# Performance work log

Measured on AMD Instinct MI355X. Metric: run time of the kernel, lower is better.

Reference implementation:

```python
import jax, jax.numpy as jnp
import numpy as np

D = 512        # input_dim
T = 64         # n_trees
DEPTH = 3
NI = 2 ** DEPTH - 1   # 7 internal nodes
NL = 2 ** DEPTH       # 8 leaves
PPT = NI * D + NI + NL * 2   # params per tree
TOT = PPT * T + T            # + tree_weights
HID = 64


def setup_inputs() -> dict:
    key = jax.random.key(0)
    ks = jax.random.split(key, 10)
    w = lambda k, s: jax.random.normal(k, s, jnp.float32) * 0.05  # xavier-ish small gain
    return {
        "X_train": jax.random.normal(ks[0], (8192, D), jnp.float32),
        "X_test": jax.random.normal(ks[1], (32768, D), jnp.float32),
        "y_train": jax.random.randint(ks[2], (8192,), 0, 2, jnp.int64),
        "W1": w(ks[3], (HID, D)), "b1": jnp.zeros(HID), "g1": jnp.ones(HID), "be1": jnp.zeros(HID),
        "W2": w(ks[4], (HID, HID)), "b2": jnp.zeros(HID),
        "H1": w(ks[5], (2 * HID, HID)), "hb1": jnp.zeros(2 * HID),
        "g2": jnp.ones(2 * HID), "be2": jnp.zeros(2 * HID),
        "H2": w(ks[6], (2 * HID, 2 * HID)), "hb2": jnp.zeros(2 * HID),
        "H3": w(ks[7], (TOT, 2 * HID)), "hb3": jnp.zeros(TOT),
    }


def _ln(x, g, b, eps=1e-5):
    m = x.mean(-1, keepdims=True)
    v = ((x - m) ** 2).mean(-1, keepdims=True)
    return (x - m) / jnp.sqrt(v + eps) * g + b


def reference(X_train, X_test, y_train, W1, b1, g1, be1, W2, b2,
              H1, hb1, g2, be2, H2, hb2, H3, hb3):
    # --- hypernet: data encoder + param generator (Dropout is eval=identity) ---
    h = jax.nn.relu(_ln(X_train @ W1.T + b1, g1, be1))
    h = jax.nn.relu(h @ W2.T + b2)
    c = h.mean(axis=0)                              # [HID] context
    u = jax.nn.relu(_ln(c @ H1.T + hb1, g2, be2))
    u = jax.nn.relu(u @ H2.T + hb2)
    params = u @ H3.T + hb3                         # [TOT]

    # --- parse per-tree params (sequential layout) ---
    rows = params[: T * PPT].reshape(T, PPT)
    sw = rows[:, : NI * D].reshape(T, NI, D)        # split weights
    sb = rows[:, NI * D: NI * D + NI]               # split bias [T, NI]
    ll = rows[:, NI * D + NI:].reshape(T, NL, 2)    # leaf logits
    tw = params[T * PPT:]                           # tree weights [T]

    # --- soft decision trees, all trees/nodes batched ---
    # sigmoid split prob for every (sample, tree, internal node); temperature=1
    p = jax.nn.sigmoid(jnp.einsum('bd,tnd->btn', X_test, sw) + sb[None])  # [B,T,NI]
    B = X_test.shape[0]
    lp = jnp.ones((B, T, 1), X_test.dtype)
    for d in range(DEPTH):                          # unrolled fixed-depth traversal
        s = 2 ** d - 1                              # heap offset of level d
        pd = p[:, :, s: s + 2 ** d]                 # [B,T,2^d]
        lp = jnp.stack([lp * (1 - pd), lp * pd], axis=-1).reshape(B, T, 2 ** (d + 1))
    # original code adds leaf contributions twice (main loop + cleanup loop)
    lp = lp * 2.0                                   # [B,T,NL]

    leaf_dist = jax.nn.softmax(ll, axis=-1)         # [T,NL,2]
    out_t = jnp.einsum('btl,tlc->btc', lp, leaf_dist)
    w = jax.nn.softmax(tw, axis=0)                  # [T]
    return jnp.einsum('btc,t->bc', out_t, w)        # [B,2]
```

## Files before the change

kernel.cpp:

```cpp
#include <hip/hip_runtime.h>
#include <hip/hip_bf16.h>

#define DD 512
#define HIDN 64
#define NTREE 64
#define NIN 7
#define PPTC 3607
#define TOTP 230912
#define SWROWS 448

typedef __attribute__((ext_vector_type(8))) short bf16x8;
typedef __attribute__((ext_vector_type(4))) float f32x4;
typedef __attribute__((ext_vector_type(8))) _Float16 h16x8;

__device__ __forceinline__ unsigned short f2bf(float f) {
  unsigned u = __float_as_uint(f);
  unsigned r = (u + 0x7FFFu + ((u >> 16) & 1u)) >> 16;
  return (unsigned short)r;
}
__device__ __forceinline__ float bf2f(unsigned short h) {
  return __uint_as_float(((unsigned)h) << 16);
}
__device__ __forceinline__ float sigmoidf_(float x) {
  return 1.0f / (1.0f + __expf(-x));
}
__device__ __forceinline__ uint2 pack_bf16x4(float4 v) {
  uint2 pk;
  pk.x = (unsigned)f2bf(v.x) | ((unsigned)f2bf(v.y) << 16);
  pk.y = (unsigned)f2bf(v.z) | ((unsigned)f2bf(v.w) << 16);
  return pk;
}

__global__ __launch_bounds__(256) void k_train(
    const float* __restrict__ Xtr, const float* __restrict__ W1,
    const float* __restrict__ b1, const float* __restrict__ g1,
    const float* __restrict__ be1, const float* __restrict__ W2,
    const float* __restrict__ b2, float* __restrict__ c_accum)
{
  __shared__ __align__(16) char smem[49408];
  char* Xc  = smem;
  char* W1c = smem + 16384;
  char* Hl  = smem + 32768;
  char* W2l = smem + 40960;
  float* cpart = (float*)(smem + 49152);

  const int tid = threadIdx.x;
  const int lane = tid & 63;
  const int wv = tid >> 6;
  const int l15 = lane & 15;
  const int gq = lane >> 4;
  const int rb0 = blockIdx.x * 64;

#pragma unroll
  for (int s = 0; s < 4; ++s) {
    int fidx = tid + s * 256;
    int n = fidx >> 4, kq = fidx & 15;
    float4 v = ((const float4*)W2)[n * 16 + kq];
    uint2 pk = pack_bf16x4(v);
    int off = n * 128 + kq * 8; off ^= (n & 7) << 4;
    *(uint2*)(W2l + off) = pk;
  }
  if (tid < 64) cpart[tid] = 0.0f;

  f32x4 acc1[4];
#pragma unroll
  for (int nt = 0; nt < 4; ++nt) { f32x4 z = {0.f,0.f,0.f,0.f}; acc1[nt] = z; }

  for (int kc = 0; kc < 4; ++kc) {
    __syncthreads();
#pragma unroll
    for (int s = 0; s < 8; ++s) {
      int idx = tid + s * 256;
      int m = idx >> 5, kq = idx & 31;
      float4 v = ((const float4*)Xtr)[(rb0 + m) * 128 + kc * 32 + kq];
      uint2 pk = pack_bf16x4(v);
      int off = m * 256 + kq * 8; off ^= (m & 7) << 4;
      *(uint2*)(Xc + off) = pk;
      float4 w = ((const float4*)W1)[m * 128 + kc * 32 + kq];
      uint2 pw = pack_bf16x4(w);
      *(uint2*)(W1c + off) = pw;
    }
    __syncthreads();
#pragma unroll
    for (int ks = 0; ks < 4; ++ks) {
      int mrow = wv * 16 + l15;
      int aoff = mrow * 256 + ks * 64 + gq * 16; aoff ^= (mrow & 7) << 4;
      bf16x8 afr = *(const bf16x8*)(Xc + aoff);
#pragma unroll
      for (int nt = 0; nt < 4; ++nt) {
        int n = nt * 16 + l15;
        int boff = n * 256 + ks * 64 + gq * 16; boff ^= (n & 7) << 4;
        bf16x8 bfr = *(const bf16x8*)(W1c + boff);
        acc1[nt] = __builtin_amdgcn_mfma_f32_16x16x32_bf16(afr, bfr, acc1[nt], 0, 0, 0);
      }
    }
  }

  float b1v[4], g1v[4], be1v[4], b2v[4];
#pragma unroll
  for (int nt = 0; nt < 4; ++nt) {
    int c = nt * 16 + l15;
    b1v[nt] = b1[c]; g1v[nt] = g1[c]; be1v[nt] = be1[c]; b2v[nt] = b2[c];
  }
  float yv[4][4], s_[4], q_[4];
#pragma unroll
  for (int i = 0; i < 4; ++i) {
    float s = 0.f, q = 0.f;
#pragma unroll
    for (int nt = 0; nt < 4; ++nt) {
      float y = acc1[nt][i] + b1v[nt];
      yv[nt][i] = y; s += y; q += y * y;
    }
    s_[i] = s; q_[i] = q;
  }
#pragma unroll
  for (int off = 1; off < 16; off <<= 1) {
#pragma unroll
    for (int i = 0; i < 4; ++i) {
      s_[i] += __shfl_xor(s_[i], off);
      q_[i] += __shfl_xor(q_[i], off);
    }
  }
  char* Hw = Hl + wv * 2048;
#pragma unroll
  for (int i = 0; i < 4; ++i) {
    float m = s_[i] * (1.0f / 64.0f);
    float var = q_[i] * (1.0f / 64.0f) - m * m;
    float rstd = rsqrtf(var + 1e-5f);
    int mrow = gq * 4 + i;
#pragma unroll
    for (int nt = 0; nt < 4; ++nt) {
      float h = (yv[nt][i] - m) * rstd * g1v[nt] + be1v[nt];
      h = fmaxf(h, 0.0f);
      int col = nt * 16 + l15;
      int off2 = mrow * 128 + col * 2; off2 ^= (mrow & 7) << 4;
      *(unsigned short*)(Hw + off2) = f2bf(h);
    }
  }
  __syncthreads();

  f32x4 acc2[4];
#pragma unroll
  for (int nt = 0; nt < 4; ++nt) { f32x4 z = {0.f,0.f,0.f,0.f}; acc2[nt] = z; }
#pragma unroll
  for (int ks = 0; ks < 2; ++ks) {
    int aoff = l15 * 128 + ks * 64 + gq * 16; aoff ^= (l15 & 7) << 4;
    bf16x8 afr = *(const bf16x8*)(Hw + aoff);
#pragma unroll
    for (int nt = 0; nt < 4; ++nt) {
      int n = nt * 16 + l15;
      int boff = n * 128 + ks * 64 + gq * 16; boff ^= (n & 7) << 4;
      bf16x8 bfr = *(const bf16x8*)(W2l + boff);
      acc2[nt] = __builtin_amdgcn_mfma_f32_16x16x32_bf16(afr, bfr, acc2[nt], 0, 0, 0);
    }
  }
  float cs[4];
#pragma unroll
  for (int nt = 0; nt < 4; ++nt) {
    float s = 0.f;
#pragma unroll
    for (int i = 0; i < 4; ++i) {
      float z = acc2[nt][i] + b2v[nt];
      s += fmaxf(z, 0.0f);
    }
    cs[nt] = s;
  }
#pragma unroll
  for (int nt = 0; nt < 4; ++nt) {
    cs[nt] += __shfl_xor(cs[nt], 16);
    cs[nt] += __shfl_xor(cs[nt], 32);
  }
  if (lane < 16) {
#pragma unroll
    for (int nt = 0; nt < 4; ++nt) atomicAdd(&cpart[nt * 16 + l15], cs[nt]);
  }
  __syncthreads();
  if (tid < 64) atomicAdd(&c_accum[tid], cpart[tid]);
}

__global__ __launch_bounds__(128) void k_head(
    const float* __restrict__ c_accum,
    const float* __restrict__ H1, const float* __restrict__ hb1,
    const float* __restrict__ g2, const float* __restrict__ be2,
    const float* __restrict__ H2, const float* __restrict__ hb2,
    float* __restrict__ u2out)
{
  __shared__ float clds[64];
  __shared__ float u1lds[128];
  __shared__ float red[4];
  int tid = threadIdx.x;
  if (tid < 64) clds[tid] = c_accum[tid] * (1.0f / 8192.0f);
  __syncthreads();
  float acc = hb1[tid];
  for (int k = 0; k < 64; ++k) acc += clds[k] * H1[tid * 64 + k];
  float s = acc, q = acc * acc;
#pragma unroll
  for (int off = 1; off < 64; off <<= 1) { s += __shfl_xor(s, off); q += __shfl_xor(q, off); }
  int wv = tid >> 6;
  if ((tid & 63) == 0) { red[wv * 2] = s; red[wv * 2 + 1] = q; }
  __syncthreads();
  float S = red[0] + red[2], Q = red[1] + red[3];
  float m = S * (1.0f / 128.0f);
  float var = Q * (1.0f / 128.0f) - m * m;
  float rstd = rsqrtf(var + 1e-5f);
  float u1 = fmaxf((acc - m) * rstd * g2[tid] + be2[tid], 0.0f);
  u1lds[tid] = u1;
  __syncthreads();
  float a2 = hb2[tid];
  for (int k = 0; k < 128; ++k) a2 += u1lds[k] * H2[tid * 128 + k];
  u2out[tid] = fmaxf(a2, 0.0f);
}

__global__ __launch_bounds__(256) void k_params(
    const float* __restrict__ H3, const float* __restrict__ hb3,
    const float* __restrict__ u2,
    unsigned short* __restrict__ Bsw, float* __restrict__ sb,
    float* __restrict__ ll, float* __restrict__ tw)
{
  __shared__ float u2l[128];
  int tid = threadIdx.x;
  if (tid < 128) u2l[tid] = u2[tid];
  __syncthreads();
  int row = blockIdx.x * 64 + (tid >> 2);
  int sub = tid & 3;
  float acc = 0.0f;
  const float4* H4 = (const float4*)H3;
#pragma unroll
  for (int j = 0; j < 8; ++j) {
    int f = j * 4 + sub;
    float4 v = H4[row * 32 + f];
    acc += v.x * u2l[f * 4] + v.y * u2l[f * 4 + 1] + v.z * u2l[f * 4 + 2] + v.w * u2l[f * 4 + 3];
  }
  acc += __shfl_xor(acc, 1);
  acc += __shfl_xor(acc, 2);
  if (sub == 0) {
    float val = acc + hb3[row];
    if (row >= 230848) {
      tw[row - 230848] = val;
    } else {
      int t = row / PPTC;
      int r = row - t * PPTC;
      if (r < 3584) {
        int n = r >> 9, d = r & 511;
        Bsw[(t * 7 + n) * 512 + d] = f2bf(val);
      } else if (r < 3591) {
        sb[t * 7 + (r - 3584)] = val;
      } else {
        ll[t * 16 + (r - 3591)] = val;
      }
    }
  }
}

__global__ __launch_bounds__(64) void k_qprep(
    const float* __restrict__ ll, const float* __restrict__ tw,
    float* __restrict__ q)
{
  int t = threadIdx.x;
  float x = tw[t];
  float m = x;
#pragma unroll
  for (int off = 1; off < 64; off <<= 1) m = fmaxf(m, __shfl_xor(m, off));
  float e = __expf(x - m);
  float s = e;
#pragma unroll
  for (int off = 1; off < 64; off <<= 1) s += __shfl_xor(s, off);
  float w = e / s;
#pragma unroll
  for (int l = 0; l < 8; ++l) {
    float a = ll[t * 16 + l * 2], b = ll[t * 16 + l * 2 + 1];
    float mm = fmaxf(a, b);
    float e0 = __expf(a - mm), e1 = __expf(b - mm);
    float inv = 2.0f * w / (e0 + e1);
    q[t * 16 + l * 2] = e0 * inv;
    q[t * 16 + l * 2 + 1] = e1 * inv;
  }
}

__global__ __launch_bounds__(512) void k_test(
    const float* __restrict__ Xt, const unsigned short* __restrict__ Bsw,
    const float* __restrict__ sb, const float* __restrict__ q,
    float* __restrict__ out)
{
  __shared__ __align__(16) char smem[39680];
  char* Xl = smem;
  char* Bl = smem + 8192;
  char* Pl = smem;
  float* sbl  = (float*)(smem + 36864);
  float* outl = (float*)(smem + 38656);

  const int tid = threadIdx.x;
  const int lane = tid & 63;
  const int wv = tid >> 6;
  const int l15 = lane & 15;
  const int gq = lane >> 4;
  const int wm = wv >> 2;
  const int wn = wv & 3;
  const int bm0 = blockIdx.x * 128;

  if (tid < 448) sbl[tid] = sb[tid];

  float qreg[16];
  {
    const float4* q4 = (const float4*)q;
#pragma unroll
    for (int j = 0; j < 4; ++j) {
      float4 v = q4[lane * 4 + j];
      qreg[j * 4] = v.x; qreg[j * 4 + 1] = v.y; qreg[j * 4 + 2] = v.z; qreg[j * 4 + 3] = v.w;
    }
  }

  const int xm = tid >> 3, xk = tid & 7;
  const int xg0 = (bm0 + xm) * 128 + xk;
  const int xg1 = (bm0 + xm + 64) * 128 + xk;
  int xo0 = xm * 64 + xk * 8;        xo0 ^= (xm & 7) << 4;
  int xo1 = (xm + 64) * 64 + xk * 8; xo1 ^= (xm & 7) << 4;

  int bg[4], bo[4];
#pragma unroll
  for (int s = 0; s < 4; ++s) {
    int idx = tid + s * 512; if (idx > 1791) idx = 1791;
    int n = idx >> 2, part = idx & 3;
    bg[s] = n * 64 + part;
    bo[s] = (n * 64 + part * 16) ^ ((n & 7) << 4);
  }

  int aoffs[4], boffs[7];
#pragma unroll
  for (int mt = 0; mt < 4; ++mt) {
    int r = wm * 64 + mt * 16 + l15;
    aoffs[mt] = (r * 64 + gq * 16) ^ ((r & 7) << 4);
  }
#pragma unroll
  for (int nt = 0; nt < 7; ++nt) {
    int r = wn * 112 + nt * 16 + l15;
    boffs[nt] = (r * 64 + gq * 16) ^ ((r & 7) << 4);
  }

  f32x4 acc[4][7];
#pragma unroll
  for (int mt = 0; mt < 4; ++mt)
#pragma unroll
    for (int nt = 0; nt < 7; ++nt) { f32x4 z = {0.f,0.f,0.f,0.f}; acc[mt][nt] = z; }

  const float4* X4 = (const float4*)Xt;
  const uint4* B4 = (const uint4*)Bsw;

  float4 xr0 = X4[xg0], xr1 = X4[xg1];
  uint4 br0 = B4[bg[0]], br1 = B4[bg[1]], br2 = B4[bg[2]], br3 = B4[bg[3]];

  for (int kt = 0; kt < 16; ++kt) {
    __syncthreads();
    *(uint2*)(Xl + xo0) = pack_bf16x4(xr0);
    *(uint2*)(Xl + xo1) = pack_bf16x4(xr1);
    *(uint4*)(Bl + bo[0]) = br0;
    *(uint4*)(Bl + bo[1]) = br1;
    *(uint4*)(Bl + bo[2]) = br2;
    *(uint4*)(Bl + bo[3]) = br3;
    if (kt < 15) {
      int k8 = (kt + 1) * 8, k4 = (kt + 1) * 4;
      xr0 = X4[xg0 + k8]; xr1 = X4[xg1 + k8];
      br0 = B4[bg[0] + k4]; br1 = B4[bg[1] + k4];
      br2 = B4[bg[2] + k4]; br3 = B4[bg[3] + k4];
    }
    __syncthreads();
    bf16x8 afr[4];
#pragma unroll
    for (int mt = 0; mt < 4; ++mt) afr[mt] = *(const bf16x8*)(Xl + aoffs[mt]);
#pragma unroll
    for (int nt = 0; nt < 7; ++nt) {
      bf16x8 bfr = *(const bf16x8*)(Bl + boffs[nt]);
#pragma unroll
      for (int mt = 0; mt < 4; ++mt)
        acc[mt][nt] = __builtin_amdgcn_mfma_f32_16x16x32_bf16(afr[mt], bfr, acc[mt][nt], 0, 0, 0);
    }
  }
  __syncthreads();

#pragma unroll
  for (int rg = 0; rg < 4; ++rg) {
    if (wm == (rg >> 1)) {
#pragma unroll
      for (int mtl = 0; mtl < 2; ++mtl) {
        const int mt = (rg & 1) * 2 + mtl;
#pragma unroll
        for (int nt = 0; nt < 7; ++nt) {
          int col = wn * 112 + nt * 16 + l15;
          float sbv = sbl[col];
          int t = col / 7;
          int j = col - t * 7;
          int slot2 = (t * 8 + j) * 2;
#pragma unroll
          for (int i = 0; i < 4; ++i) {
            int rl = mtl * 16 + gq * 4 + i;
            float p = sigmoidf_(acc[mt][nt][i] + sbv);
            *(_Float16*)(Pl + rl * 1024 + slot2) = (_Float16)p;
          }
        }
      }
    }
    __syncthreads();
#pragma unroll
    for (int k = 0; k < 4; ++k) {
      int rl = wv * 4 + k;
      h16x8 v = *(const h16x8*)(Pl + rl * 1024 + lane * 16);
      float p0 = (float)v[0], p1 = (float)v[1], p2 = (float)v[2];
      float p3 = (float)v[3], p4 = (float)v[4], p5 = (float)v[5], p6 = (float)v[6];
      float n0 = 1.f - p0, n1 = 1.f - p1, n2 = 1.f - p2;
      float a00 = n0 * n1, a01 = n0 * p1, a10 = p0 * n2, a11 = p0 * p2;
      float L0 = a00 * (1.f - p3), L1 = a00 * p3;
      float L2 = a01 * (1.f - p4), L3 = a01 * p4;
      float L4 = a10 * (1.f - p5), L5 = a10 * p5;
      float L6 = a11 * (1.f - p6), L7 = a11 * p6;
      float o0 = L0*qreg[0] + L1*qreg[2] + L2*qreg[4] + L3*qreg[6]
               + L4*qreg[8] + L5*qreg[10] + L6*qreg[12] + L7*qreg[14];
      float o1 = L0*qreg[1] + L1*qreg[3] + L2*qreg[5] + L3*qreg[7]
               + L4*qreg[9] + L5*qreg[11] + L6*qreg[13] + L7*qreg[15];
#pragma unroll
      for (int off = 1; off < 64; off <<= 1) {
        o0 += __shfl_xor(o0, off);
        o1 += __shfl_xor(o1, off);
      }
      if (lane == 0) {
        int gr = rg * 32 + rl;
        outl[gr * 2] = o0;
        outl[gr * 2 + 1] = o1;
      }
    }
    __syncthreads();
  }
  if (tid < 256) out[bm0 * 2 + tid] = outl[tid];
}

extern "C" void kernel_launch(void* const* d_in, const int* in_sizes, int n_in,
                              void* d_out, int out_size, void* d_ws, size_t ws_size,
                              hipStream_t stream)
{
  const float* Xtr = (const float*)d_in[0];
  const float* Xte = (const float*)d_in[1];
  const float* W1  = (const float*)d_in[3];
  const float* b1  = (const float*)d_in[4];
  const float* g1  = (const float*)d_in[5];
  const float* be1 = (const float*)d_in[6];
  const float* W2  = (const float*)d_in[7];
  const float* b2  = (const float*)d_in[8];
  const float* H1  = (const float*)d_in[9];
  const float* hb1 = (const float*)d_in[10];
  const float* g2  = (const float*)d_in[11];
  const float* be2 = (const float*)d_in[12];
  const float* H2  = (const float*)d_in[13];
  const float* hb2 = (const float*)d_in[14];
  const float* H3  = (const float*)d_in[15];
  const float* hb3 = (const float*)d_in[16];
  float* out = (float*)d_out;
  char* ws = (char*)d_ws;

  float* c_accum = (float*)ws;
  float* u2      = (float*)(ws + 256);
  float* sb      = (float*)(ws + 768);
  float* ll      = (float*)(ws + 2560);
  float* tw      = (float*)(ws + 6656);
  float* q       = (float*)(ws + 6912);
  unsigned short* Bsw = (unsigned short*)(ws + 11008);

  hipMemsetAsync(c_accum, 0, 64 * sizeof(float), stream);
  k_train<<<128, 256, 0, stream>>>(Xtr, W1, b1, g1, be1, W2, b2, c_accum);
  k_head<<<1, 128, 0, stream>>>(c_accum, H1, hb1, g2, be2, H2, hb2, u2);
  k_params<<<3608, 256, 0, stream>>>(H3, hb3, u2, Bsw, sb, ll, tw);
  k_qprep<<<1, 64, 0, stream>>>(ll, tw, q);
  k_test<<<256, 512, 0, stream>>>(Xte, Bsw, sb, q, out);
}
```

Measured before the change: 96.29 us.

## Double-buffer test GEMM LDS, split train kernel over more blocks, drop atomics

The test GEMM kernel now uses two LDS buffers so the next K-tile's global loads and stores overlap the MFMA work on the current tile, at the cost of roughly double the shared memory per block. The train encoder kernel processes 32 rows per block across 256 blocks with a 2x2 wave split and register prefetch of the next K chunk. It writes per-block partial context sums instead of using atomics, which removes the memset. The head kernel reduces those partials and uses four accumulators in its dot products. Higher LDS use in k_test may lower occupancy.

```diff
diff --git a/kernel.cpp b/kernel.cpp
--- a/kernel.cpp
+++ b/kernel.cpp
@@ -18,9 +18,6 @@
   unsigned r = (u + 0x7FFFu + ((u >> 16) & 1u)) >> 16;
   return (unsigned short)r;
 }
-__device__ __forceinline__ float bf2f(unsigned short h) {
-  return __uint_as_float(((unsigned)h) << 16);
-}
 __device__ __forceinline__ float sigmoidf_(float x) {
   return 1.0f / (1.0f + __expf(-x));
 }
@@ -35,21 +32,27 @@
     const float* __restrict__ Xtr, const float* __restrict__ W1,
     const float* __restrict__ b1, const float* __restrict__ g1,
     const float* __restrict__ be1, const float* __restrict__ W2,
-    const float* __restrict__ b2, float* __restrict__ c_accum)
+    const float* __restrict__ b2, float* __restrict__ c_part)
 {
-  __shared__ __align__(16) char smem[49408];
+  __shared__ __align__(16) char smem[37888];
   char* Xc  = smem;
-  char* W1c = smem + 16384;
-  char* Hl  = smem + 32768;
-  char* W2l = smem + 40960;
-  float* cpart = (float*)(smem + 49152);
+  char* W1c = smem + 8192;
+  char* Hl  = smem + 24576;
+  char* W2l = smem + 28672;
+  float* lnb = (float*)(smem + 36864);
+  float* cp  = (float*)(smem + 37376);
 
   const int tid = threadIdx.x;
   const int lane = tid & 63;
   const int wv = tid >> 6;
   const int l15 = lane & 15;
   const int gq = lane >> 4;
-  const int rb0 = blockIdx.x * 64;
+  const int wm = wv >> 1;
+  const int wn = wv & 1;
+  const int rb0 = blockIdx.x * 32;
+
+  const float4* X4g = (const float4*)Xtr;
+  const float4* W4g = (const float4*)W1;
 
 #pragma unroll
   for (int s = 0; s < 4; ++s) {
@@ -60,54 +63,75 @@
     int off = n * 128 + kq * 8; off ^= (n & 7) << 4;
     *(uint2*)(W2l + off) = pk;
   }
-  if (tid < 64) cpart[tid] = 0.0f;
-
-  f32x4 acc1[4];
-#pragma unroll
-  for (int nt = 0; nt < 4; ++nt) { f32x4 z = {0.f,0.f,0.f,0.f}; acc1[nt] = z; }
+
+  int xga[4], xo[4];
+#pragma unroll
+  for (int s = 0; s < 4; ++s) {
+    int f = tid + s * 256;
+    int m = f >> 5, kq = f & 31;
+    xga[s] = (rb0 + m) * 128 + kq;
+    xo[s] = (m * 256 + kq * 8) ^ ((m & 7) << 4);
+  }
+  int wga[8], wo[8];
+#pragma unroll
+  for (int s = 0; s < 8; ++s) {
+    int f = tid + s * 256;
+    int n = f >> 5, kq = f & 31;
+    wga[s] = n * 128 + kq;
+    wo[s] = (n * 256 + kq * 8) ^ ((n & 7) << 4);
+  }
+
+  f32x4 acc1[2];
+#pragma unroll
+  for (int nt = 0; nt < 2; ++nt) { f32x4 z = {0.f,0.f,0.f,0.f}; acc1[nt] = z; }
+
+  float4 xr[4], wr[8];
+#pragma unroll
+  for (int s = 0; s < 4; ++s) xr[s] = X4g[xga[s]];
+#pragma unroll
+  for (int s = 0; s < 8; ++s) wr[s] = W4g[wga[s]];
 
   for (int kc = 0; kc < 4; ++kc) {
     __syncthreads();
 #pragma unroll
-    for (int s = 0; s < 8; ++s) {
-      int idx = tid + s * 256;
-      int m = idx >> 5, kq = idx & 31;
-      float4 v = ((const float4*)Xtr)[(rb0 + m) * 128 + kc * 32 + kq];
-      uint2 pk = pack_bf16x4(v);
-      int off = m * 256 + kq * 8; off ^= (m & 7) << 4;
-      *(uint2*)(Xc + off) = pk;
-      float4 w = ((const float4*)W1)[m * 128 + kc * 32 + kq];
-      uint2 pw = pack_bf16x4(w);
-      *(uint2*)(W1c + off) = pw;
+    for (int s = 0; s < 4; ++s) *(uint2*)(Xc + xo[s]) = pack_bf16x4(xr[s]);
+#pragma unroll
+    for (int s = 0; s < 8; ++s) *(uint2*)(W1c + wo[s]) = pack_bf16x4(wr[s]);
+    if (kc < 3) {
+      int ko = (kc + 1) * 32;
+#pragma unroll
+      for (int s = 0; s < 4; ++s) xr[s] = X4g[xga[s] + ko];
+#pragma unroll
+      for (int s = 0; s < 8; ++s) wr[s] = W4g[wga[s] + ko];
     }
     __syncthreads();
 #pragma unroll
     for (int ks = 0; ks < 4; ++ks) {
-      int mrow = wv * 16 + l15;
-      int aoff = mrow * 256 + ks * 64 + gq * 16; aoff ^= (mrow & 7) << 4;
+      int arow = wm * 16 + l15;
+      int aoff = (arow * 256 + ks * 64 + gq * 16) ^ ((arow & 7) << 4);
       bf16x8 afr = *(const bf16x8*)(Xc + aoff);
 #pragma unroll
-      for (int nt = 0; nt < 4; ++nt) {
-        int n = nt * 16 + l15;
-        int boff = n * 256 + ks * 64 + gq * 16; boff ^= (n & 7) << 4;
+      for (int nt = 0; nt < 2; ++nt) {
+        int brow = wn * 32 + nt * 16 + l15;
+        int boff = (brow * 256 + ks * 64 + gq * 16) ^ ((brow & 7) << 4);
         bf16x8 bfr = *(const bf16x8*)(W1c + boff);
         acc1[nt] = __builtin_amdgcn_mfma_f32_16x16x32_bf16(afr, bfr, acc1[nt], 0, 0, 0);
       }
     }
   }
 
-  float b1v[4], g1v[4], be1v[4], b2v[4];
-#pragma unroll
-  for (int nt = 0; nt < 4; ++nt) {
-    int c = nt * 16 + l15;
+  float b1v[2], g1v[2], be1v[2], b2v[2];
+#pragma unroll
+  for (int nt = 0; nt < 2; ++nt) {
+    int c = wn * 32 + nt * 16 + l15;
     b1v[nt] = b1[c]; g1v[nt] = g1[c]; be1v[nt] = be1[c]; b2v[nt] = b2[c];
   }
-  float yv[4][4], s_[4], q_[4];
+  float yv[2][4], s_[4], q_[4];
 #pragma unroll
   for (int i = 0; i < 4; ++i) {
     float s = 0.f, q = 0.f;
 #pragma unroll
-    for (int nt = 0; nt < 4; ++nt) {
+    for (int nt = 0; nt < 2; ++nt) {
       float y = acc1[nt][i] + b1v[nt];
       yv[nt][i] = y; s += y; q += y * y;
     }
@@ -121,65 +145,74 @@
       q_[i] += __shfl_xor(q_[i], off);
     }
   }
-  char* Hw = Hl + wv * 2048;
+  if (l15 == 0) {
+#pragma unroll
+    for (int i = 0; i < 4; ++i) {
+      int row = wm * 16 + gq * 4 + i;
+      float2 sv; sv.x = s_[i]; sv.y = q_[i];
+      *(float2*)(lnb + (row * 2 + wn) * 2) = sv;
+    }
+  }
+  __syncthreads();
 #pragma unroll
   for (int i = 0; i < 4; ++i) {
-    float m = s_[i] * (1.0f / 64.0f);
-    float var = q_[i] * (1.0f / 64.0f) - m * m;
+    int row = wm * 16 + gq * 4 + i;
+    float2 e0 = *(float2*)(lnb + (row * 2 + 0) * 2);
+    float2 e1 = *(float2*)(lnb + (row * 2 + 1) * 2);
+    float m = (e0.x + e1.x) * (1.0f / 64.0f);
+    float var = (e0.y + e1.y) * (1.0f / 64.0f) - m * m;
     float rstd = rsqrtf(var + 1e-5f);
-    int mrow = gq * 4 + i;
-#pragma unroll
-    for (int nt = 0; nt < 4; ++nt) {
+#pragma unroll
+    for (int nt = 0; nt < 2; ++nt) {
       float h = (yv[nt][i] - m) * rstd * g1v[nt] + be1v[nt];
       h = fmaxf(h, 0.0f);
-      int col = nt * 16 + l15;
-      int off2 = mrow * 128 + col * 2; off2 ^= (mrow & 7) << 4;
-      *(unsigned short*)(Hw + off2) = f2bf(h);
-    }
-  }
-  __syncthreads();
-
-  f32x4 acc2[4];
-#pragma unroll
-  for (int nt = 0; nt < 4; ++nt) { f32x4 z = {0.f,0.f,0.f,0.f}; acc2[nt] = z; }
+      int col = wn * 32 + nt * 16 + l15;
+      int off2 = (row * 128 + col * 2) ^ ((row & 7) << 4);
+      *(unsigned short*)(Hl + off2) = f2bf(h);
+    }
+  }
+  __syncthreads();
+
+  f32x4 acc2[2];
+#pragma unroll
+  for (int nt = 0; nt < 2; ++nt) { f32x4 z = {0.f,0.f,0.f,0.f}; acc2[nt] = z; }
 #pragma unroll
   for (int ks = 0; ks < 2; ++ks) {
-    int aoff = l15 * 128 + ks * 64 + gq * 16; aoff ^= (l15 & 7) << 4;
-    bf16x8 afr = *(const bf16x8*)(Hw + aoff);
-#pragma unroll
-    for (int nt = 0; nt < 4; ++nt) {
-      int n = nt * 16 + l15;
-      int boff = n * 128 + ks * 64 + gq * 16; boff ^= (n & 7) << 4;
+    int arow = wm * 16 + l15;
+    int aoff = (arow * 128 + ks * 64 + gq * 16) ^ ((arow & 7) << 4);
+    bf16x8 afr = *(const bf16x8*)(Hl + aoff);
+#pragma unroll
+    for (int nt = 0; nt < 2; ++nt) {
+      int brow = wn * 32 + nt * 16 + l15;
+      int boff = (brow * 128 + ks * 64 + gq * 16) ^ ((brow & 7) << 4);
       bf16x8 bfr = *(const bf16x8*)(W2l + boff);
       acc2[nt] = __builtin_amdgcn_mfma_f32_16x16x32_bf16(afr, bfr, acc2[nt], 0, 0, 0);
     }
   }
-  float cs[4];
-#pragma unroll
-  for (int nt = 0; nt < 4; ++nt) {
+  float cs[2];
+#pragma unroll
+  for (int nt = 0; nt < 2; ++nt) {
     float s = 0.f;
 #pragma unroll
-    for (int i = 0; i < 4; ++i) {
-      float z = acc2[nt][i] + b2v[nt];
-      s += fmaxf(z, 0.0f);
-    }
+    for (int i = 0; i < 4; ++i) s += fmaxf(acc2[nt][i] + b2v[nt], 0.0f);
     cs[nt] = s;
   }
 #pragma unroll
-  for (int nt = 0; nt < 4; ++nt) {
+  for (int nt = 0; nt < 2; ++nt) {
     cs[nt] += __shfl_xor(cs[nt], 16);
     cs[nt] += __shfl_xor(cs[nt], 32);
   }
   if (lane < 16) {
 #pragma unroll
-    for (int nt = 0; nt < 4; ++nt) atomicAdd(&cpart[nt * 16 + l15], cs[nt]);
-  }
-  __syncthreads();
-  if (tid < 64) atomicAdd(&c_accum[tid], cpart[tid]);
+    for (int nt = 0; nt < 2; ++nt)
+      cp[wm * 64 + wn * 32 + nt * 16 + lane] = cs[nt];
+  }
+  __syncthreads();
+  if (tid < 64) c_part[blockIdx.x * 64 + tid] = cp[tid] + cp[64 + tid];
 }
 
 __global__ __launch_bounds__(128) void k_head(
-    const float* __restrict__ c_accum,
+    const float* __restrict__ c_part,
     const float* __restrict__ H1, const float* __restrict__ hb1,
     const float* __restrict__ g2, const float* __restrict__ be2,
     const float* __restrict__ H2, const float* __restrict__ hb2,
@@ -189,10 +222,25 @@
   __shared__ float u1lds[128];
   __shared__ float red[4];
   int tid = threadIdx.x;
-  if (tid < 64) clds[tid] = c_accum[tid] * (1.0f / 8192.0f);
-  __syncthreads();
-  float acc = hb1[tid];
-  for (int k = 0; k < 64; ++k) acc += clds[k] * H1[tid * 64 + k];
+  if (tid < 64) {
+    float s0 = 0.f, s1 = 0.f, s2 = 0.f, s3 = 0.f;
+    for (int b = 0; b < 256; b += 4) {
+      s0 += c_part[(b + 0) * 64 + tid];
+      s1 += c_part[(b + 1) * 64 + tid];
+      s2 += c_part[(b + 2) * 64 + tid];
+      s3 += c_part[(b + 3) * 64 + tid];
+    }
+    clds[tid] = (s0 + s1 + s2 + s3) * (1.0f / 8192.0f);
+  }
+  __syncthreads();
+  float a0 = 0.f, a1 = 0.f, a2p = 0.f, a3 = 0.f;
+  for (int k = 0; k < 64; k += 4) {
+    a0 += clds[k + 0] * H1[tid * 64 + k + 0];
+    a1 += clds[k + 1] * H1[tid * 64 + k + 1];
+    a2p += clds[k + 2] * H1[tid * 64 + k + 2];
+    a3 += clds[k + 3] * H1[tid * 64 + k + 3];
+  }
+  float acc = hb1[tid] + ((a0 + a1) + (a2p + a3));
   float s = acc, q = acc * acc;
 #pragma unroll
   for (int off = 1; off < 64; off <<= 1) { s += __shfl_xor(s, off); q += __shfl_xor(q, off); }
@@ -206,9 +254,14 @@
   float u1 = fmaxf((acc - m) * rstd * g2[tid] + be2[tid], 0.0f);
   u1lds[tid] = u1;
   __syncthreads();
-  float a2 = hb2[tid];
-  for (int k = 0; k < 128; ++k) a2 += u1lds[k] * H2[tid * 128 + k];
-  u2out[tid] = fmaxf(a2, 0.0f);
+  float c0 = 0.f, c1 = 0.f, c2 = 0.f, c3 = 0.f;
+  for (int k = 0; k < 128; k += 4) {
+    c0 += u1lds[k + 0] * H2[tid * 128 + k + 0];
+    c1 += u1lds[k + 1] * H2[tid * 128 + k + 1];
+    c2 += u1lds[k + 2] * H2[tid * 128 + k + 2];
+    c3 += u1lds[k + 3] * H2[tid * 128 + k + 3];
+  }
+  u2out[tid] = fmaxf(hb2[tid] + ((c0 + c1) + (c2 + c3)), 0.0f);
 }
 
 __global__ __launch_bounds__(256) void k_params(
@@ -282,12 +335,14 @@
     const float* __restrict__ sb, const float* __restrict__ q,
     float* __restrict__ out)
 {
-  __shared__ __align__(16) char smem[39680];
-  char* Xl = smem;
-  char* Bl = smem + 8192;
-  char* Pl = smem;
-  float* sbl  = (float*)(smem + 36864);
-  float* outl = (float*)(smem + 38656);
+  __shared__ __align__(16) char smem[76544];
+  char* Xb0 = smem;
+  char* Xb1 = smem + 8192;
+  char* Bb0 = smem + 16384;
+  char* Bb1 = smem + 45056;
+  char* Pl  = smem + 16384;
+  float* sbl  = (float*)(smem + 73728);
+  float* outl = (float*)(smem + 75520);
 
   const int tid = threadIdx.x;
   const int lane = tid & 63;
@@ -297,6 +352,7 @@
   const int wm = wv >> 2;
   const int wn = wv & 3;
   const int bm0 = blockIdx.x * 128;
+  const bool btail = (tid < 256);
 
   if (tid < 448) sbl[tid] = sb[tid];
 
@@ -313,13 +369,13 @@
   const int xm = tid >> 3, xk = tid & 7;
   const int xg0 = (bm0 + xm) * 128 + xk;
   const int xg1 = (bm0 + xm + 64) * 128 + xk;
-  int xo0 = xm * 64 + xk * 8;        xo0 ^= (xm & 7) << 4;
-  int xo1 = (xm + 64) * 64 + xk * 8; xo1 ^= (xm & 7) << 4;
+  const int xo0 = (xm * 64 + xk * 8) ^ ((xm & 7) << 4);
+  const int xo1 = ((xm + 64) * 64 + xk * 8) ^ ((xm & 7) << 4);
 
   int bg[4], bo[4];
 #pragma unroll
   for (int s = 0; s < 4; ++s) {
-    int idx = tid + s * 512; if (idx > 1791) idx = 1791;
+    int idx = tid + s * 512;
     int n = idx >> 2, part = idx & 3;
     bg[s] = n * 64 + part;
     bo[s] = (n * 64 + part * 16) ^ ((n & 7) << 4);
@@ -346,36 +402,57 @@
   const float4* X4 = (const float4*)Xt;
   const uint4* B4 = (const uint4*)Bsw;
 
-  float4 xr0 = X4[xg0], xr1 = X4[xg1];
-  uint4 br0 = B4[bg[0]], br1 = B4[bg[1]], br2 = B4[bg[2]], br3 = B4[bg[3]];
-
-  for (int kt = 0; kt < 16; ++kt) {
+#define LOADX(xa, xb, kt) do { xa = X4[xg0 + (kt) * 8]; xb = X4[xg1 + (kt) * 8]; } while (0)
+#define LOADB(b0_, b1_, b2_, b3_, kt) do { \
+    b0_ = B4[bg[0] + (kt) * 4]; b1_ = B4[bg[1] + (kt) * 4]; b2_ = B4[bg[2] + (kt) * 4]; \
+    if (btail) b3_ = B4[bg[3] + (kt) * 4]; } while (0)
+#define STORET(Xb, Bb, xa, xb, b0_, b1_, b2_, b3_) do { \
+    *(uint2*)((Xb) + xo0) = pack_bf16x4(xa); \
+    *(uint2*)((Xb) + xo1) = pack_bf16x4(xb); \
+    *(uint4*)((Bb) + bo[0]) = b0_; \
+    *(uint4*)((Bb) + bo[1]) = b1_; \
+    *(uint4*)((Bb) + bo[2]) = b2_; \
+    if (btail) *(uint4*)((Bb) + bo[3]) = b3_; } while (0)
+#define COMPUTE(Xb, Bb) do { \
+    bf16x8 afr[4]; \
+    _Pragma("unroll") \
+    for (int mt = 0; mt < 4; ++mt) afr[mt] = *(const bf16x8*)((Xb) + aoffs[mt]); \
+    _Pragma("unroll") \
+    for (int nt = 0; nt < 7; ++nt) { \
+      bf16x8 bfr = *(const bf16x8*)((Bb) + boffs[nt]); \
+      _Pragma("unroll") \
+      for (int mt = 0; mt < 4; ++mt) \
+        acc[mt][nt] = __builtin_amdgcn_mfma_f32_16x16x32_bf16(afr[mt], bfr, acc[mt][nt], 0, 0, 0); \
+    } } while (0)
+
+  float4 xra, xrb, xca, xcb;
+  uint4 ba0, ba1, ba2, ba3, bb0, bb1, bb2, bb3;
+
+  LOADX(xra, xca, 0);
+  LOADB(ba0, ba1, ba2, ba3, 0);
+  STORET(Xb0, Bb0, xra, xca, ba0, ba1, ba2, ba3);
+  LOADX(xrb, xcb, 1);
+  LOADB(bb0, bb1, bb2, bb3, 1);
+  __syncthreads();
+
+  for (int kt2 = 0; kt2 < 16; kt2 += 2) {
+    STORET(Xb1, Bb1, xrb, xcb, bb0, bb1, bb2, bb3);
+    if (kt2 + 2 < 16) {
+      LOADX(xra, xca, kt2 + 2);
+      LOADB(ba0, ba1, ba2, ba3, kt2 + 2);
+    }
+    COMPUTE(Xb0, Bb0);
     __syncthreads();
-    *(uint2*)(Xl + xo0) = pack_bf16x4(xr0);
-    *(uint2*)(Xl + xo1) = pack_bf16x4(xr1);
-    *(uint4*)(Bl + bo[0]) = br0;
-    *(uint4*)(Bl + bo[1]) = br1;
-    *(uint4*)(Bl + bo[2]) = br2;
-    *(uint4*)(Bl + bo[3]) = br3;
-    if (kt < 15) {
-      int k8 = (kt + 1) * 8, k4 = (kt + 1) * 4;
-      xr0 = X4[xg0 + k8]; xr1 = X4[xg1 + k8];
-      br0 = B4[bg[0] + k4]; br1 = B4[bg[1] + k4];
-      br2 = B4[bg[2] + k4]; br3 = B4[bg[3] + k4];
-    }
+    if (kt2 + 2 < 16) {
+      STORET(Xb0, Bb0, xra, xca, ba0, ba1, ba2, ba3);
+      if (kt2 + 3 < 16) {
+        LOADX(xrb, xcb, kt2 + 3);
+        LOADB(bb0, bb1, bb2, bb3, kt2 + 3);
+      }
+    }
+    COMPUTE(Xb1, Bb1);
     __syncthreads();
-    bf16x8 afr[4];
-#pragma unroll
-    for (int mt = 0; mt < 4; ++mt) afr[mt] = *(const bf16x8*)(Xl + aoffs[mt]);
-#pragma unroll
-    for (int nt = 0; nt < 7; ++nt) {
-      bf16x8 bfr = *(const bf16x8*)(Bl + boffs[nt]);
-#pragma unroll
-      for (int mt = 0; mt < 4; ++mt)
-        acc[mt][nt] = __builtin_amdgcn_mfma_f32_16x16x32_bf16(afr[mt], bfr, acc[mt][nt], 0, 0, 0);
-    }
-  }
-  __syncthreads();
+  }
 
 #pragma unroll
   for (int rg = 0; rg < 4; ++rg) {
@@ -430,6 +507,10 @@
     __syncthreads();
   }
   if (tid < 256) out[bm0 * 2 + tid] = outl[tid];
+#undef LOADX
+#undef LOADB
+#undef STORET
+#undef COMPUTE
 }
 
 extern "C" void kernel_launch(void* const* d_in, const int* in_sizes, int n_in,
@@ -455,17 +536,16 @@
   float* out = (float*)d_out;
   char* ws = (char*)d_ws;
 
-  float* c_accum = (float*)ws;
-  float* u2      = (float*)(ws + 256);
-  float* sb      = (float*)(ws + 768);
-  float* ll      = (float*)(ws + 2560);
-  float* tw      = (float*)(ws + 6656);
-  float* q       = (float*)(ws + 6912);
-  unsigned short* Bsw = (unsigned short*)(ws + 11008);
-
-  hipMemsetAsync(c_accum, 0, 64 * sizeof(float), stream);
-  k_train<<<128, 256, 0, stream>>>(Xtr, W1, b1, g1, be1, W2, b2, c_accum);
-  k_head<<<1, 128, 0, stream>>>(c_accum, H1, hb1, g2, be2, H2, hb2, u2);
+  float* c_part = (float*)ws;
+  float* u2     = (float*)(ws + 65536);
+  float* sb     = (float*)(ws + 66048);
+  float* ll     = (float*)(ws + 67840);
+  float* tw     = (float*)(ws + 71936);
+  float* q      = (float*)(ws + 72192);
+  unsigned short* Bsw = (unsigned short*)(ws + 76288);
+
+  k_train<<<256, 256, 0, stream>>>(Xtr, W1, b1, g1, be1, W2, b2, c_part);
+  k_head<<<1, 128, 0, stream>>>(c_part, H1, hb1, g2, be2, H2, hb2, u2);
   k_params<<<3608, 256, 0, stream>>>(H3, hb3, u2, Bsw, sb, ll, tw);
   k_qprep<<<1, 64, 0, stream>>>(ll, tw, q);
   k_test<<<256, 512, 0, stream>>>(Xte, Bsw, sb, q, out);
```

Measured after the change: 84.87 us. 11.9% less time.
